# Optimization experiments

Measured on AMD Instinct MI355X. Metric: run time of the kernel, lower is better.

## Reference

```python
import jax, jax.numpy as jnp
import numpy as np

HEADS = 16
EPS = 1e-5  # nn.LayerNorm default


def setup_inputs() -> dict:
    key = jax.random.key(0)
    ks = jax.random.split(key, 3)
    b, n, dim = 4, 1024, 1024
    x = jax.random.normal(ks[0], (b, n, dim), jnp.float32)
    ln_gamma = jnp.ones((dim,), jnp.float32)
    ln_beta = jnp.zeros((dim,), jnp.float32)
    # torch.nn.Linear stores weight as [out_features, in_features]
    w_qkv = jax.random.normal(ks[1], (3 * dim, dim), jnp.float32) * (dim ** -0.5)
    w_out = jax.random.normal(ks[2], (dim, dim), jnp.float32) * (dim ** -0.5)
    b_out = jnp.zeros((dim,), jnp.float32)
    return {"x": x, "ln_gamma": ln_gamma, "ln_beta": ln_beta,
            "w_qkv": w_qkv, "w_out": w_out, "b_out": b_out, "topk": 32}


def reference(x, ln_gamma, ln_beta, w_qkv, w_out, b_out, topk):
    b, n, dim = x.shape
    h = HEADS
    d = dim // h
    scale = d ** -0.5  # (inner_dim/heads)^-0.5 with inner_dim=dim

    # LayerNorm (biased variance, matching torch)
    mu = x.mean(-1, keepdims=True)
    var = x.var(-1, keepdims=True)
    xn = (x - mu) * jax.lax.rsqrt(var + EPS) * ln_gamma + ln_beta

    # qkv projection (no bias): y = x @ W^T
    qkv = jnp.einsum('bnd,ed->bne', xn, w_qkv)  # [b, n, 3*dim]
    q, k, v = jnp.split(qkv, 3, axis=-1)
    split_heads = lambda t: t.reshape(b, n, h, d).transpose(0, 2, 1, 3)  # [b,h,n,d]
    q = split_heads(q) * scale
    k = split_heads(k)
    v = split_heads(v)

    sim = jnp.einsum('bhid,bhjd->bhij', q, k)          # [b,h,n,n]
    attn = jax.nn.softmax(sim, axis=-1)
    # top-k SELECTION: probability values are discarded, only indices used
    _, idx = jax.lax.top_k(attn, topk)                 # [b,h,n,topk]
    # gather v rows at top-k indices and sum (unweighted), matching
    # torch.gather(vv, 2, idx).sum(-2)
    gathered = jnp.take_along_axis(
        v, idx.reshape(b, h, n * topk)[..., None], axis=2)  # [b,h,n*topk,d]
    xsum = gathered.reshape(b, h, n, topk, d).sum(axis=3)   # [b,h,n,d]

    # global min/max normalization then exp
    xmin = xsum.min()
    xmax = xsum.max()
    out = jnp.exp((xsum - xmin) / (xmax - xmin))

    out = out.transpose(0, 2, 1, 3).reshape(b, n, dim)  # b h n d -> b n (h d)
    # final projection (self.out Linear; Dropout(0.2) inert at eval)
    return jnp.einsum('bnd,ed->bne', out, w_out) + b_out
```

## Files before the change

### kernel.cpp

```cpp
#include <hip/hip_runtime.h>


#define LN_EPS 1e-5f

using half8   = __attribute__((ext_vector_type(8))) _Float16;
using half4   = __attribute__((ext_vector_type(4))) _Float16;
using float4v = __attribute__((ext_vector_type(4))) float;

__device__ __forceinline__ void gload_lds16(const void* g, void* l) {
  __builtin_amdgcn_global_load_lds(
      (const __attribute__((address_space(1))) void*)g,
      (__attribute__((address_space(3))) void*)l, 16, 0, 0);
}
__device__ __forceinline__ float4v mfma16(half8 a, half8 b, float4v c) {
  return __builtin_amdgcn_mfma_f32_16x16x32_f16(a, b, c, 0, 0, 0);
}
struct HL { _Float16 h, l; };
__device__ __forceinline__ HL split2(float x) {
  _Float16 h = (_Float16)x;
  return { h, (_Float16)(x - (float)h) };
}
__device__ __forceinline__ int mbcnt(unsigned long long m) {
  return __builtin_amdgcn_mbcnt_hi((unsigned)(m >> 32),
         __builtin_amdgcn_mbcnt_lo((unsigned)m, 0u));
}

__device__ __forceinline__ unsigned fkey(float f) {
  unsigned u = __float_as_uint(f);
  return ((int)u < 0) ? ~u : (u | 0x80000000u);
}
__device__ __forceinline__ int enc_i(float f) {
  int i = __float_as_int(f);
  return i >= 0 ? i : (i ^ 0x7fffffff);
}
__device__ __forceinline__ float dec_i(int e) {
  return __int_as_float(e >= 0 ? e : (e ^ 0x7fffffff));
}

__global__ __launch_bounds__(256)
void prep_kernel(const float* __restrict__ x, const float* __restrict__ gamma,
                 const float* __restrict__ beta,
                 _Float16* __restrict__ xh, _Float16* __restrict__ xl,
                 const float* __restrict__ wqkv, const float* __restrict__ wout,
                 _Float16* __restrict__ wqh, _Float16* __restrict__ wql,
                 _Float16* __restrict__ woh,
                 int* __restrict__ pmin, int* __restrict__ pmax) {
  int blk = blockIdx.x, t = threadIdx.x;
  if (blk < 4096) {
    __shared__ float red[8];
    int row = blk;
    const float4* xr = (const float4*)(x + (size_t)row * 1024);
    float4 v = xr[t];
    float s  = v.x + v.y + v.z + v.w;
    float s2 = v.x*v.x + v.y*v.y + v.z*v.z + v.w*v.w;
    #pragma unroll
    for (int o = 32; o >= 1; o >>= 1) {
      s  += __shfl_xor(s,  o, 64);
      s2 += __shfl_xor(s2, o, 64);
    }
    int w = t >> 6, l = t & 63;
    if (l == 0) { red[w*2] = s; red[w*2+1] = s2; }
    __syncthreads();
    float S  = red[0] + red[2] + red[4] + red[6];
    float S2 = red[1] + red[3] + red[5] + red[7];
    float mu  = S * (1.0f/1024.0f);
    float var = S2 * (1.0f/1024.0f) - mu*mu;
    float r = rsqrtf(var + LN_EPS);
    float4 g  = ((const float4*)gamma)[t];
    float4 bb = ((const float4*)beta)[t];
    float o0 = (v.x - mu) * r * g.x + bb.x;
    float o1 = (v.y - mu) * r * g.y + bb.y;
    float o2 = (v.z - mu) * r * g.z + bb.z;
    float o3 = (v.w - mu) * r * g.w + bb.w;
    HL r0 = split2(o0), r1 = split2(o1), r2 = split2(o2), r3 = split2(o3);
    half4 hh = { r0.h, r1.h, r2.h, r3.h };
    half4 ll = { r0.l, r1.l, r2.l, r3.l };
    size_t e = (size_t)row * 1024 + t*4;
    *(half4*)(xh + e) = hh;
    *(half4*)(xl + e) = ll;
  } else if (blk < 8192) {
    size_t i4 = (size_t)(blk - 4096) * 256 + t;
    if (i4 < 786432) {
      float4 v = ((const float4*)wqkv)[i4];
      HL r0 = split2(v.x), r1 = split2(v.y), r2 = split2(v.z), r3 = split2(v.w);
      half4 hh = { r0.h, r1.h, r2.h, r3.h };
      half4 ll = { r0.l, r1.l, r2.l, r3.l };
      ((half4*)wqh)[i4] = hh;
      ((half4*)wql)[i4] = ll;
    } else {
      size_t off = i4 - 786432;
      float4 v = ((const float4*)wout)[off];
      half4 hh = { (_Float16)v.x, (_Float16)v.y, (_Float16)v.z, (_Float16)v.w };
      ((half4*)woh)[off] = hh;
    }
  } else {
    if (t < 64)              pmin[t]      = 0x7fffffff;
    else if (t < 128)        pmax[t - 64] = (int)0x80000000;
  }
}

__global__ __launch_bounds__(256)
void gemm_qkv(const _Float16* __restrict__ Ah, const _Float16* __restrict__ Al,
              const _Float16* __restrict__ Bh, const _Float16* __restrict__ Bl,
              _Float16* __restrict__ QH, _Float16* __restrict__ QL,
              _Float16* __restrict__ KH, _Float16* __restrict__ KL,
              float* __restrict__ CV) {
  __shared__ __align__(16) _Float16 lds[4 * 128 * 32];
  const int K = 1024;
  int tid = threadIdx.x, w = tid >> 6, l = tid & 63;
  int m0 = blockIdx.y * 128, n0 = blockIdx.x * 128;
  int wm = (w >> 1) * 64, wn = (w & 1) * 64;

  const _Float16* src = (w == 0) ? Ah : (w == 1) ? Al : (w == 2) ? Bh : Bl;
  int rowbase = (w < 2) ? m0 : n0;
  _Float16* dst = lds + (size_t)w * 4096;
  int sr = l >> 2, sc = l & 3;

  float4v acc[4][4];
  #pragma unroll
  for (int u = 0; u < 4; ++u)
    #pragma unroll
    for (int vv = 0; vv < 4; ++vv) acc[u][vv] = (float4v){0.f, 0.f, 0.f, 0.f};

  int quad = l >> 4, lo16 = l & 15;
  for (int kt = 0; kt < K; kt += 32) {
    __syncthreads();
    #pragma unroll
    for (int i = 0; i < 8; ++i) {
      int row = i * 16 + sr;
      gload_lds16(src + (size_t)(rowbase + row) * K + kt + sc * 8,
                  dst + row * 32 + sc * 8);
    }
    __syncthreads();
    half8 ah[4], al[4], bh[4], bl[4];
    #pragma unroll
    for (int u = 0; u < 4; ++u) {
      int mrow = wm + u * 16 + lo16;
      int nrow = wn + u * 16 + lo16;
      ah[u] = *(const half8*)&lds[        (size_t)mrow * 32 + quad * 8];
      al[u] = *(const half8*)&lds[ 4096 + (size_t)mrow * 32 + quad * 8];
      bh[u] = *(const half8*)&lds[ 8192 + (size_t)nrow * 32 + quad * 8];
      bl[u] = *(const half8*)&lds[12288 + (size_t)nrow * 32 + quad * 8];
    }
    #pragma unroll
    for (int u = 0; u < 4; ++u)
      #pragma unroll
      for (int vv = 0; vv < 4; ++vv)
        acc[u][vv] = mfma16(ah[u], bh[vv], acc[u][vv]);
    #pragma unroll
    for (int u = 0; u < 4; ++u)
      #pragma unroll
      for (int vv = 0; vv < 4; ++vv)
        acc[u][vv] = mfma16(ah[u], bl[vv], acc[u][vv]);
    #pragma unroll
    for (int u = 0; u < 4; ++u)
      #pragma unroll
      for (int vv = 0; vv < 4; ++vv)
        acc[u][vv] = mfma16(al[u], bh[vv], acc[u][vv]);
  }

  #pragma unroll
  for (int u = 0; u < 4; ++u) {
    #pragma unroll
    for (int vv = 0; vv < 4; ++vv) {
      #pragma unroll
      for (int rg = 0; rg < 4; ++rg) {
        int row = m0 + wm + u * 16 + quad * 4 + rg;
        int col = n0 + wn + vv * 16 + lo16;
        float val = acc[u][vv][rg];
        int which = col >> 10, h = (col >> 6) & 15, dd = col & 63;
        int b = row >> 10, i = row & 1023;
        size_t e = ((size_t)(b * 16 + h) << 16) + ((size_t)i << 6) + dd;
        if (which == 2) { CV[e] = val; }
        else {
          HL sp = split2(val);
          if (which == 0) { QH[e] = sp.h; QL[e] = sp.l; }
          else            { KH[e] = sp.h; KL[e] = sp.l; }
        }
      }
    }
  }
}

__global__ __launch_bounds__(1024)
void attn_kernel(const _Float16* __restrict__ qh, const _Float16* __restrict__ ql,
                 const _Float16* __restrict__ kh, const _Float16* __restrict__ kl,
                 const float* __restrict__ vg, float* __restrict__ xsum,
                 int* __restrict__ pmin, int* __restrict__ pmax) {
  __shared__ float simb[16][1028];
  __shared__ int sel[16][32];
  __shared__ float bmn[16], bmx[16];
  int g = blockIdx.x;
  int xcd = g & 7, slot = g >> 3;
  int bh = (slot >> 6) * 8 + xcd, grp = slot & 63;
  int tid = threadIdx.x, w = tid >> 6, l = tid & 63;
  int quad = l >> 4, lo16 = l & 15;
  size_t hb = (size_t)bh << 16;

  const _Float16* qhp = qh + hb + ((size_t)(grp * 16 + lo16) << 6);
  const _Float16* qlp = ql + hb + ((size_t)(grp * 16 + lo16) << 6);
  half8 ah0 = *(const half8*)(qhp + quad * 8);
  half8 ah1 = *(const half8*)(qhp + 32 + quad * 8);
  half8 al0 = *(const half8*)(qlp + quad * 8);
  half8 al1 = *(const half8*)(qlp + 32 + quad * 8);

  const _Float16* khp = kh + hb;
  const _Float16* klp = kl + hb;
  int jbase = w * 64;

  half8 b0, b1, c0, c1, d0, d1, e0, e1;
  {
    size_t off = ((size_t)(jbase + lo16) << 6) + quad * 8;
    b0 = *(const half8*)(khp + off);
    b1 = *(const half8*)(khp + off + 32);
    c0 = *(const half8*)(klp + off);
    c1 = *(const half8*)(klp + off + 32);
  }
  #pragma unroll
  for (int tt = 0; tt < 4; ++tt) {
    if (tt < 3) {
      size_t off = ((size_t)(jbase + (tt + 1) * 16 + lo16) << 6) + quad * 8;
      d0 = *(const half8*)(khp + off);
      d1 = *(const half8*)(khp + off + 32);
      e0 = *(const half8*)(klp + off);
      e1 = *(const half8*)(klp + off + 32);
    }
    float4v acc = (float4v){0.f, 0.f, 0.f, 0.f};
    acc = mfma16(ah0, b0, acc);
    acc = mfma16(ah0, c0, acc);
    acc = mfma16(al0, b0, acc);
    acc = mfma16(ah1, b1, acc);
    acc = mfma16(ah1, c1, acc);
    acc = mfma16(al1, b1, acc);
    int jc = jbase + tt * 16 + lo16;
    #pragma unroll
    for (int rg = 0; rg < 4; ++rg)
      simb[quad * 4 + rg][jc] = acc[rg];
    b0 = d0; b1 = d1; c0 = e0; c1 = e1;
  }
  __syncthreads();

  unsigned ku[16];
  #pragma unroll
  for (int s = 0; s < 16; ++s) ku[s] = fkey(simb[w][s * 64 + l]);

  unsigned cur = 0u;
  bool exact = false;
  for (int bit = 31; bit >= 0; --bit) {
    unsigned T = cur | (1u << bit);
    int c = 0;
    #pragma unroll
    for (int s = 0; s < 16; ++s) c += __popcll(__ballot(ku[s] >= T));
    if (c >= 32) {
      cur = T;
      if (c == 32) { exact = true; break; }
    }
  }

  int base = 0;
  if (exact) {
    #pragma unroll
    for (int s = 0; s < 16; ++s) {
      bool take = ku[s] >= cur;
      unsigned long long mtk = __ballot(take);
      if (take) sel[w][base + mbcnt(mtk)] = s * 64 + l;
      base += __popcll(mtk);
    }
  } else {
    int gcnt = 0;
    #pragma unroll
    for (int s = 0; s < 16; ++s) gcnt += __popcll(__ballot(ku[s] > cur));
    int need = 32 - gcnt;
    int eqb = 0;
    #pragma unroll
    for (int s = 0; s < 16; ++s) {
      bool gt = ku[s] > cur;
      bool eq = ku[s] == cur;
      unsigned long long meq = __ballot(eq);
      int eqr = eqb + mbcnt(meq);
      bool take = gt || (eq && (eqr < need));
      unsigned long long mtk = __ballot(take);
      if (take) sel[w][base + mbcnt(mtk)] = s * 64 + l;
      base += __popcll(mtk);
      eqb  += __popcll(meq);
    }
  }

  const float* vb = vg + hb;
  int lg = l >> 4, lc = (l & 15) * 4;
  float4 vacc = {0.f, 0.f, 0.f, 0.f};
  #pragma unroll
  for (int p = 0; p < 8; ++p) {
    int j = sel[w][p * 4 + lg];
    float4 t = *(const float4*)(vb + ((size_t)j << 6) + lc);
    vacc.x += t.x; vacc.y += t.y; vacc.z += t.z; vacc.w += t.w;
  }
  #pragma unroll
  for (int o = 32; o >= 16; o >>= 1) {
    vacc.x += __shfl_xor(vacc.x, o, 64);
    vacc.y += __shfl_xor(vacc.y, o, 64);
    vacc.z += __shfl_xor(vacc.z, o, 64);
    vacc.w += __shfl_xor(vacc.w, o, 64);
  }
  if (l < 16)
    *(float4*)(xsum + hb + ((size_t)(grp * 16 + w) << 6) + l * 4) = vacc;

  float m4 = fminf(fminf(vacc.x, vacc.y), fminf(vacc.z, vacc.w));
  float M4 = fmaxf(fmaxf(vacc.x, vacc.y), fmaxf(vacc.z, vacc.w));
  #pragma unroll
  for (int o = 8; o >= 1; o >>= 1) {
    m4 = fminf(m4, __shfl_xor(m4, o, 64));
    M4 = fmaxf(M4, __shfl_xor(M4, o, 64));
  }
  if (l == 0) { bmn[w] = m4; bmx[w] = M4; }
  __syncthreads();
  if (w == 0 && l < 16) {
    float a = bmn[l], b2 = bmx[l];
    #pragma unroll
    for (int o = 8; o >= 1; o >>= 1) {
      a  = fminf(a,  __shfl_xor(a,  o, 64));
      b2 = fmaxf(b2, __shfl_xor(b2, o, 64));
    }
    if (l == 0) {
      atomicMin(pmin + bh, enc_i(a));
      atomicMax(pmax + bh, enc_i(b2));
    }
  }
}

__global__ __launch_bounds__(256)
void fin_kernel(const float* __restrict__ xsum, const int* __restrict__ pmin,
                const int* __restrict__ pmax, _Float16* __restrict__ oh) {
  __shared__ float mm[2];
  int tid = threadIdx.x;
  if (tid < 64) {
    float fa = dec_i(pmin[tid]);
    float fb = dec_i(pmax[tid]);
    #pragma unroll
    for (int o = 32; o >= 1; o >>= 1) {
      fa = fminf(fa, __shfl_xor(fa, o, 64));
      fb = fmaxf(fb, __shfl_xor(fb, o, 64));
    }
    if (tid == 0) { mm[0] = fa; mm[1] = fb; }
  }
  __syncthreads();
  float mn = mm[0];
  float inv = 1.0f / (mm[1] - mn);
  int idx = blockIdx.x * 256 + tid;
  float4 xv = ((const float4*)xsum)[idx];
  half4 hh = { (_Float16)expf((xv.x - mn) * inv),
               (_Float16)expf((xv.y - mn) * inv),
               (_Float16)expf((xv.z - mn) * inv),
               (_Float16)expf((xv.w - mn) * inv) };
  int e0 = idx << 2;
  int bh = e0 >> 16, i = (e0 >> 6) & 1023, dd = e0 & 63;
  int b = bh >> 4, h = bh & 15;
  size_t oe = ((size_t)(b * 1024 + i) << 10) + (h << 6) + dd;
  *(half4*)(oh + oe) = hh;
}

__global__ __launch_bounds__(256)
void gemm_out(const _Float16* __restrict__ A, const _Float16* __restrict__ Bw,
              const float* __restrict__ bias, float* __restrict__ CO) {
  __shared__ __align__(16) _Float16 lds[192 * 32];
  const int K = 1024;
  int tid = threadIdx.x, w = tid >> 6, l = tid & 63;
  int m0 = blockIdx.y * 128, n0 = blockIdx.x * 64;
  int wm = (w >> 1) * 64, wn = (w & 1) * 32;
  int sr = l >> 2, sc = l & 3;
  int quad = l >> 4, lo16 = l & 15;

  float4v acc[4][2];
  #pragma unroll
  for (int u = 0; u < 4; ++u)
    #pragma unroll
    for (int vv = 0; vv < 2; ++vv) acc[u][vv] = (float4v){0.f, 0.f, 0.f, 0.f};

  for (int kt = 0; kt < K; kt += 32) {
    __syncthreads();
    #pragma unroll
    for (int i = 0; i < 3; ++i) {
      int row = w * 48 + i * 16 + sr;
      const _Float16* sp = (row < 128)
          ? A  + (size_t)(m0 + row) * K + kt + sc * 8
          : Bw + (size_t)(n0 + row - 128) * K + kt + sc * 8;
      gload_lds16(sp, lds + row * 32 + sc * 8);
    }
    __syncthreads();
    half8 af[4], bf[2];
    #pragma unroll
    for (int u = 0; u < 4; ++u)
      af[u] = *(const half8*)&lds[(size_t)(wm + u * 16 + lo16) * 32 + quad * 8];
    #pragma unroll
    for (int vv = 0; vv < 2; ++vv)
      bf[vv] = *(const half8*)&lds[(size_t)(128 + wn + vv * 16 + lo16) * 32
                                   + quad * 8];
    #pragma unroll
    for (int u = 0; u < 4; ++u)
      #pragma unroll
      for (int vv = 0; vv < 2; ++vv)
        acc[u][vv] = mfma16(af[u], bf[vv], acc[u][vv]);
  }

  #pragma unroll
  for (int u = 0; u < 4; ++u) {
    #pragma unroll
    for (int vv = 0; vv < 2; ++vv) {
      #pragma unroll
      for (int rg = 0; rg < 4; ++rg) {
        int row = m0 + wm + u * 16 + quad * 4 + rg;
        int col = n0 + wn + vv * 16 + lo16;
        CO[(size_t)row * 1024 + col] = acc[u][vv][rg] + bias[col];
      }
    }
  }
}

extern "C" void kernel_launch(void* const* d_in, const int* in_sizes, int n_in,
                              void* d_out, int out_size, void* d_ws, size_t ws_size,
                              hipStream_t stream) {
  const float* x     = (const float*)d_in[0];
  const float* gamma = (const float*)d_in[1];
  const float* beta  = (const float*)d_in[2];
  const float* w_qkv = (const float*)d_in[3];
  const float* w_out = (const float*)d_in[4];
  const float* b_out = (const float*)d_in[5];

  char* B = (char*)d_ws;
  const size_t MB = 1024ull * 1024ull;
  float*    v   = (float*)B;
  _Float16* qh  = (_Float16*)(B + 16*MB);
  _Float16* ql  = (_Float16*)(B + 24*MB);
  _Float16* kh  = (_Float16*)(B + 32*MB);
  _Float16* kl  = (_Float16*)(B + 40*MB);
  float*    xs  = (float*)(B + 48*MB);
  _Float16* xh  = (_Float16*)(B + 48*MB);
  _Float16* xl  = (_Float16*)(B + 56*MB);
  _Float16* woh = (_Float16*)(B + 64*MB);
  int*     pmin = (int*)(B + 66*MB);
  int*     pmax = (int*)(B + 66*MB + 4096);
  _Float16* wqh = (_Float16*)(B + 69*MB);
  _Float16* wql = (_Float16*)(B + 75*MB);
  _Float16* oth = qh;

  prep_kernel<<<8193, 256, 0, stream>>>(x, gamma, beta, xh, xl,
                                        w_qkv, w_out, wqh, wql, woh,
                                        pmin, pmax);
  gemm_qkv<<<dim3(24, 32), 256, 0, stream>>>(
      xh, xl, wqh, wql, qh, ql, kh, kl, v);
  attn_kernel<<<4096, 1024, 0, stream>>>(qh, ql, kh, kl, v, xs, pmin, pmax);
  fin_kernel<<<4096, 256, 0, stream>>>(xs, pmin, pmax, oth);
  gemm_out<<<dim3(16, 32), 256, 0, stream>>>(oth, woh, b_out, (float*)d_out);
}
```

Measured before the change: 387.6 us.

## Narrow top-k radix search with wave max/min prefix and radix-4 steps

```diff
diff --git a/kernel.cpp b/kernel.cpp
--- a/kernel.cpp
+++ b/kernel.cpp
@@ -187,7 +187,7 @@
                  const _Float16* __restrict__ kh, const _Float16* __restrict__ kl,
                  const float* __restrict__ vg, float* __restrict__ xsum,
                  int* __restrict__ pmin, int* __restrict__ pmax) {
-  __shared__ float simb[16][1028];
+  __shared__ unsigned kb[16][1028];
   __shared__ int sel[16][32];
   __shared__ float bmn[16], bmx[16];
   int g = blockIdx.x;
@@ -235,24 +235,52 @@
     int jc = jbase + tt * 16 + lo16;
     #pragma unroll
     for (int rg = 0; rg < 4; ++rg)
-      simb[quad * 4 + rg][jc] = acc[rg];
+      kb[quad * 4 + rg][jc] = fkey(acc[rg]);
     b0 = d0; b1 = d1; c0 = e0; c1 = e1;
   }
   __syncthreads();
 
   unsigned ku[16];
   #pragma unroll
-  for (int s = 0; s < 16; ++s) ku[s] = fkey(simb[w][s * 64 + l]);
-
-  unsigned cur = 0u;
+  for (int s = 0; s < 16; ++s) ku[s] = kb[w][s * 64 + l];
+
+  unsigned lmax = ku[0];
+  #pragma unroll
+  for (int s = 1; s < 16; ++s) lmax = (ku[s] > lmax) ? ku[s] : lmax;
+  unsigned rmx = lmax, rmn = lmax;
+  #pragma unroll
+  for (int o = 32; o >= 1; o >>= 1) {
+    unsigned tx = (unsigned)__shfl_xor((int)rmx, o, 64);
+    unsigned tn = (unsigned)__shfl_xor((int)rmn, o, 64);
+    rmx = (tx > rmx) ? tx : rmx;
+    rmn = (tn < rmn) ? tn : rmn;
+  }
+
+  unsigned cur;
   bool exact = false;
-  for (int bit = 31; bit >= 0; --bit) {
-    unsigned T = cur | (1u << bit);
-    int c = 0;
-    #pragma unroll
-    for (int s = 0; s < 16; ++s) c += __popcll(__ballot(ku[s] >= T));
-    if (c >= 32) {
-      cur = T;
+  unsigned diff = rmx ^ rmn;
+  if (diff == 0u) {
+    cur = rmx;
+  } else {
+    int hbit = 31 - __builtin_clz(diff);
+    unsigned mask = (hbit == 31) ? 0xffffffffu : ((2u << hbit) - 1u);
+    cur = rmx & ~mask;
+    for (int p = hbit >> 1; p >= 0; --p) {
+      int sh = p + p;
+      unsigned T1 = cur | (1u << sh);
+      unsigned T2 = cur | (2u << sh);
+      unsigned T3 = cur | (3u << sh);
+      int c1 = 0, c2 = 0, c3 = 0;
+      #pragma unroll
+      for (int s = 0; s < 16; ++s) {
+        c1 += __popcll(__ballot(ku[s] >= T1));
+        c2 += __popcll(__ballot(ku[s] >= T2));
+        c3 += __popcll(__ballot(ku[s] >= T3));
+      }
+      int c = -1;
+      if (c1 >= 32) { cur = T1; c = c1; }
+      if (c2 >= 32) { cur = T2; c = c2; }
+      if (c3 >= 32) { cur = T3; c = c3; }
       if (c == 32) { exact = true; break; }
     }
   }
```

Result: slower. 491.7 us (+26.9%).

## Replace radix bit-search top-k with lane-max threshold filter and rank-by-count selection

Applied to the files above, without the earlier changes.

```diff
diff --git a/kernel.cpp b/kernel.cpp
--- a/kernel.cpp
+++ b/kernel.cpp
@@ -187,7 +187,7 @@
                  const _Float16* __restrict__ kh, const _Float16* __restrict__ kl,
                  const float* __restrict__ vg, float* __restrict__ xsum,
                  int* __restrict__ pmin, int* __restrict__ pmax) {
-  __shared__ float simb[16][1028];
+  __shared__ __align__(16) unsigned kb[16][1028];
   __shared__ int sel[16][32];
   __shared__ float bmn[16], bmx[16];
   int g = blockIdx.x;
@@ -208,13 +208,13 @@
   const _Float16* klp = kl + hb;
   int jbase = w * 64;
 
-  half8 b0, b1, c0, c1, d0, d1, e0, e1;
+  half8 b0, b1, c0f, c1f, d0, d1, e0, e1;
   {
     size_t off = ((size_t)(jbase + lo16) << 6) + quad * 8;
-    b0 = *(const half8*)(khp + off);
-    b1 = *(const half8*)(khp + off + 32);
-    c0 = *(const half8*)(klp + off);
-    c1 = *(const half8*)(klp + off + 32);
+    b0  = *(const half8*)(khp + off);
+    b1  = *(const half8*)(khp + off + 32);
+    c0f = *(const half8*)(klp + off);
+    c1f = *(const half8*)(klp + off + 32);
   }
   #pragma unroll
   for (int tt = 0; tt < 4; ++tt) {
@@ -227,62 +227,115 @@
     }
     float4v acc = (float4v){0.f, 0.f, 0.f, 0.f};
     acc = mfma16(ah0, b0, acc);
-    acc = mfma16(ah0, c0, acc);
+    acc = mfma16(ah0, c0f, acc);
     acc = mfma16(al0, b0, acc);
     acc = mfma16(ah1, b1, acc);
-    acc = mfma16(ah1, c1, acc);
+    acc = mfma16(ah1, c1f, acc);
     acc = mfma16(al1, b1, acc);
     int jc = jbase + tt * 16 + lo16;
     #pragma unroll
     for (int rg = 0; rg < 4; ++rg)
-      simb[quad * 4 + rg][jc] = acc[rg];
-    b0 = d0; b1 = d1; c0 = e0; c1 = e1;
+      kb[quad * 4 + rg][jc] = fkey(acc[rg]);
+    b0 = d0; b1 = d1; c0f = e0; c1f = e1;
   }
   __syncthreads();
 
   unsigned ku[16];
   #pragma unroll
-  for (int s = 0; s < 16; ++s) ku[s] = fkey(simb[w][s * 64 + l]);
-
-  unsigned cur = 0u;
-  bool exact = false;
-  for (int bit = 31; bit >= 0; --bit) {
-    unsigned T = cur | (1u << bit);
-    int c = 0;
-    #pragma unroll
-    for (int s = 0; s < 16; ++s) c += __popcll(__ballot(ku[s] >= T));
-    if (c >= 32) {
-      cur = T;
-      if (c == 32) { exact = true; break; }
-    }
-  }
-
-  int base = 0;
-  if (exact) {
+  for (int s = 0; s < 16; ++s) ku[s] = kb[w][s * 64 + l];
+
+  unsigned lmax = ku[0];
+  #pragma unroll
+  for (int s = 1; s < 16; ++s) lmax = (ku[s] > lmax) ? ku[s] : lmax;
+  unsigned LB = lmax;
+  #pragma unroll
+  for (int o = 32; o >= 1; o >>= 1) {
+    unsigned t = (unsigned)__shfl_xor((int)LB, o, 64);
+    LB = (t < LB) ? t : LB;
+  }
+
+  int cl = 0;
+  #pragma unroll
+  for (int s = 0; s < 16; ++s) cl += (ku[s] >= LB) ? 1 : 0;
+  int scan = cl;
+  #pragma unroll
+  for (int o = 1; o < 64; o <<= 1) {
+    int t = __shfl_up(scan, o, 64);
+    if (l >= o) scan += t;
+  }
+  int N = __shfl(scan, 63, 64);
+  int cbase = scan - cl;
+
+  if (N <= 128) {
+    unsigned long long* cb = (unsigned long long*)&kb[w][0];
+    int pos = cbase;
     #pragma unroll
     for (int s = 0; s < 16; ++s) {
-      bool take = ku[s] >= cur;
-      unsigned long long mtk = __ballot(take);
-      if (take) sel[w][base + mbcnt(mtk)] = s * 64 + l;
-      base += __popcll(mtk);
-    }
+      if (ku[s] >= LB) {
+        cb[pos] = ((unsigned long long)ku[s] << 10)
+                  | (unsigned)(1023 - (s * 64 + l));
+        ++pos;
+      }
+    }
+    if (l == 0) { cb[N] = 0ull; cb[N + 1] = 0ull; cb[N + 2] = 0ull; }
+
+    unsigned long long m0c = cb[l];
+    bool h1 = (64 + l) < N;
+    unsigned long long m1c = h1 ? cb[64 + l] : 0ull;
+
+    int r0a = 0, r0b = 0, r1a = 0, r1b = 0;
+    int N4 = (N + 3) & ~3;
+    for (int j = 0; j < N4; j += 4) {
+      unsigned long long a0 = cb[j + 0], a1 = cb[j + 1];
+      unsigned long long a2 = cb[j + 2], a3 = cb[j + 3];
+      r0a += (a0 > m0c); r1a += (a0 > m1c);
+      r0b += (a1 > m0c); r1b += (a1 > m1c);
+      r0a += (a2 > m0c); r1a += (a2 > m1c);
+      r0b += (a3 > m0c); r1b += (a3 > m1c);
+    }
+    int r0 = r0a + r0b, r1 = r1a + r1b;
+    if (r0 < 32)       sel[w][r0] = 1023 - (int)(m0c & 1023ull);
+    if (h1 && r1 < 32) sel[w][r1] = 1023 - (int)(m1c & 1023ull);
   } else {
-    int gcnt = 0;
-    #pragma unroll
-    for (int s = 0; s < 16; ++s) gcnt += __popcll(__ballot(ku[s] > cur));
-    int need = 32 - gcnt;
-    int eqb = 0;
-    #pragma unroll
-    for (int s = 0; s < 16; ++s) {
-      bool gt = ku[s] > cur;
-      bool eq = ku[s] == cur;
-      unsigned long long meq = __ballot(eq);
-      int eqr = eqb + mbcnt(meq);
-      bool take = gt || (eq && (eqr < need));
-      unsigned long long mtk = __ballot(take);
-      if (take) sel[w][base + mbcnt(mtk)] = s * 64 + l;
-      base += __popcll(mtk);
-      eqb  += __popcll(meq);
+    unsigned cur = 0u;
+    bool exact = false;
+    for (int bit = 31; bit >= 0; --bit) {
+      unsigned T = cur | (1u << bit);
+      int c = 0;
+      #pragma unroll
+      for (int s = 0; s < 16; ++s) c += __popcll(__ballot(ku[s] >= T));
+      if (c >= 32) {
+        cur = T;
+        if (c == 32) { exact = true; break; }
+      }
+    }
+    int base = 0;
+    if (exact) {
+      #pragma unroll
+      for (int s = 0; s < 16; ++s) {
+        bool take = ku[s] >= cur;
+        unsigned long long mtk = __ballot(take);
+        if (take) sel[w][base + mbcnt(mtk)] = s * 64 + l;
+        base += __popcll(mtk);
+      }
+    } else {
+      int gcnt = 0;
+      #pragma unroll
+      for (int s = 0; s < 16; ++s) gcnt += __popcll(__ballot(ku[s] > cur));
+      int need = 32 - gcnt;
+      int eqb = 0;
+      #pragma unroll
+      for (int s = 0; s < 16; ++s) {
+        bool gt = ku[s] > cur;
+        bool eq = ku[s] == cur;
+        unsigned long long meq = __ballot(eq);
+        int eqr = eqb + mbcnt(meq);
+        bool take = gt || (eq && (eqr < need));
+        unsigned long long mtk = __ballot(take);
+        if (take) sel[w][base + mbcnt(mtk)] = s * 64 + l;
+        base += __popcll(mtk);
+        eqb  += __popcll(meq);
+      }
     }
   }
 
```

Result: slower. 597.3 us (+54.1%).
